# Optimization experiments

Hardware: AMD Instinct MI355X
Metric: run time of the kernel (lower is better)

## Reference

```python
import jax, jax.numpy as jnp
import numpy as np

B, L, D, I = 4, 4096, 2048, 5632


def setup_inputs() -> dict:
    key = jax.random.key(0)
    ks = jax.random.split(key, 8)
    s = 0.02  # weight init scale
    return {
        "hidden_states": jax.random.normal(ks[0], (B, L, D), dtype=jnp.float32),
        "gen_token_mask": jax.random.bernoulli(ks[1], 0.5, (B, L)),
        "und_gate": jax.random.normal(ks[2], (D, I), dtype=jnp.float32) * s,
        "und_up": jax.random.normal(ks[3], (D, I), dtype=jnp.float32) * s,
        "und_down": jax.random.normal(ks[4], (I, D), dtype=jnp.float32) * s,
        "gen_gate": jax.random.normal(ks[5], (D, I), dtype=jnp.float32) * s,
        "gen_up": jax.random.normal(ks[6], (D, I), dtype=jnp.float32) * s,
        "gen_down": jax.random.normal(ks[7], (I, D), dtype=jnp.float32) * s,
    }


def _swiglu_mlp(x, w_gate, w_up, w_down):
    # Qwen2MLP: down_proj(silu(gate_proj(x)) * up_proj(x)), no biases
    return jnp.einsum("bli,id->bld", jax.nn.silu(jnp.einsum("bld,di->bli", x, w_gate)) * jnp.einsum("bld,di->bli", x, w_up), w_down)


def reference(hidden_states, gen_token_mask, und_gate, und_up, und_down, gen_gate, gen_up, gen_down):
    # moe_forward: tokens with mask=True go to gen expert, others to und expert.
    # The torch code does gather->expert->scatter; the math is a per-token select
    # between the two experts' outputs, expressed here jit-compatibly as a where.
    und_out = _swiglu_mlp(hidden_states, und_gate, und_up, und_down)
    gen_out = _swiglu_mlp(hidden_states, gen_gate, gen_up, gen_down)
    return jnp.where(gen_token_mask[..., None], gen_out, und_out)
```

## Files before the change

### kernel.cpp

```cpp
#include <hip/hip_runtime.h>
#include <stdint.h>

#define D_DIM 2048
#define I_DIM 5632
#define NTOK  16384
#define MROWS 16512
#define MTILES 129
#define CH0   65
#define CH1   64
#define HROWS (CH0 * 128)

using f32x4  = __attribute__((ext_vector_type(4))) float;
using bf16x8 = __attribute__((ext_vector_type(8))) __bf16;
using u16x8  = __attribute__((ext_vector_type(8))) unsigned short;
using u16x4  = __attribute__((ext_vector_type(4))) unsigned short;
typedef unsigned short ushort;

__device__ __forceinline__ ushort f2bf(float f) {
  union { float f; unsigned int u; } v; v.f = f;
  unsigned int r = v.u + 0x7fffu + ((v.u >> 16) & 1u);
  return (ushort)(r >> 16);
}

__device__ __forceinline__ void glds16(const void* g, void* l) {
  __builtin_amdgcn_global_load_lds(
      (__attribute__((address_space(1))) void*)(g),
      (__attribute__((address_space(3))) void*)(l),
      16, 0, 0);
}

__global__ void count_kernel(const int* __restrict__ mask, int* __restrict__ cnt) {
  int i = blockIdx.x * 256 + threadIdx.x;
  if (i < NTOK && mask[i] == 0) atomicAdd(&cnt[0], 1);
}

__global__ void assign_kernel(const int* __restrict__ mask, int* __restrict__ cnt,
                              int* __restrict__ rowmap) {
  int i = blockIdx.x * 256 + threadIdx.x;
  if (i >= NTOK) return;
  int n0  = cnt[0];
  int n0p = (n0 + 127) & ~127;
  int row;
  if (mask[i] == 0) row = atomicAdd(&cnt[1], 1);
  else              row = n0p + atomicAdd(&cnt[2], 1);
  rowmap[row] = i;
}

__global__ __launch_bounds__(256) void cast_x_kernel(const float* __restrict__ in,
                                                     ushort* __restrict__ out) {
  int i = blockIdx.x * 256 + threadIdx.x;
  f32x4 v = ((const f32x4*)in)[i];
  u16x4 o;
#pragma unroll
  for (int j = 0; j < 4; j++) o[j] = f2bf(v[j]);
  ((u16x4*)out)[i] = o;
}

__global__ __launch_bounds__(256) void transpose_cast_kernel(
    const float* __restrict__ in, ushort* __restrict__ out, int R, int C) {
  __shared__ ushort s[64][72];
  int tC = blockIdx.x, tR = blockIdx.y;
  int tid = threadIdx.x;
  int r0 = tid >> 4;
  int c4 = (tid & 15) * 4;
  const float* src = in + (size_t)(tR * 64 + r0) * C + tC * 64 + c4;
#pragma unroll
  for (int rr = 0; rr < 64; rr += 16) {
    f32x4 v = *(const f32x4*)(src + (size_t)rr * C);
#pragma unroll
    for (int j = 0; j < 4; j++) s[r0 + rr][c4 + j] = f2bf(v[j]);
  }
  __syncthreads();
  int r8 = tid >> 3;
  int c8 = (tid & 7) * 8;
#pragma unroll
  for (int rr = 0; rr < 64; rr += 32) {
    int orow = r8 + rr;
    u16x8 v;
#pragma unroll
    for (int j = 0; j < 8; j++) v[j] = s[c8 + j][orow];
    *(u16x8*)(out + (size_t)(tC * 64 + orow) * R + tR * 64 + c8) = v;
  }
}

__global__ __launch_bounds__(256, 2)
void gateup_kernel(const ushort* __restrict__ x, const int* __restrict__ rowmap,
                   const int* __restrict__ cnt, const ushort* __restrict__ wt,
                   ushort* __restrict__ h, int mbase) {
  __shared__ ushort sA[128 * 64];
  __shared__ ushort sG[128 * 64];
  __shared__ ushort sU[128 * 64];

  const int bn = blockIdx.x, bm = blockIdx.y;
  const int gtile = mbase + bm;
  const int tid = threadIdx.x;
  const int lane = tid & 63, wave = tid >> 6;
  const int wm = (wave & 1) * 64, wn = (wave >> 1) * 64;
  const int lrow = lane & 15, quad = lane >> 4;

  const int n0p = (cnt[0] + 127) & ~127;
  const int grp = (gtile * 128 >= n0p) ? 1 : 0;
  const size_t WSZ = (size_t)I_DIM * D_DIM;
  const ushort* Wg = wt + (size_t)(grp * 2) * WSZ;
  const ushort* Wu = Wg + WSZ;

  const ushort *aP[4], *gP[4], *uP[4];
#pragma unroll
  for (int is = 0; is < 4; is++) {
    int g = is * 256 + tid;
    int r = g >> 3, c = g & 7;
    int cs = c ^ (r & 7);
    int tok = rowmap[gtile * 128 + r];
    if (tok < 0) tok = 0;
    aP[is] = x  + (size_t)tok * D_DIM + cs * 8;
    gP[is] = Wg + (size_t)(bn * 128 + r) * D_DIM + cs * 8;
    uP[is] = Wu + (size_t)(bn * 128 + r) * D_DIM + cs * 8;
  }

  f32x4 accG[4][4], accU[4][4];
#pragma unroll
  for (int i = 0; i < 4; i++)
#pragma unroll
    for (int j = 0; j < 4; j++) {
      accG[i][j] = (f32x4){0.f, 0.f, 0.f, 0.f};
      accU[i][j] = (f32x4){0.f, 0.f, 0.f, 0.f};
    }

  for (int k0 = 0; k0 < D_DIM; k0 += 64) {
#pragma unroll
    for (int is = 0; is < 4; is++) {
      int wbase = (is * 256 + wave * 64) * 8;
      glds16(aP[is] + k0, &sA[wbase]);
      glds16(gP[is] + k0, &sG[wbase]);
      glds16(uP[is] + k0, &sU[wbase]);
    }
    __syncthreads();
#pragma unroll
    for (int kk = 0; kk < 2; kk++) {
      const int co = ((kk * 4 + quad) ^ (lane & 7)) * 8;
      bf16x8 af[4], gf[4], uf[4];
#pragma unroll
      for (int i = 0; i < 4; i++) af[i] = *(const bf16x8*)&sA[(wm + i * 16 + lrow) * 64 + co];
#pragma unroll
      for (int j = 0; j < 4; j++) gf[j] = *(const bf16x8*)&sG[(wn + j * 16 + lrow) * 64 + co];
#pragma unroll
      for (int j = 0; j < 4; j++) uf[j] = *(const bf16x8*)&sU[(wn + j * 16 + lrow) * 64 + co];
#pragma unroll
      for (int i = 0; i < 4; i++)
#pragma unroll
        for (int j = 0; j < 4; j++) {
          accG[i][j] = __builtin_amdgcn_mfma_f32_16x16x32_bf16(af[i], gf[j], accG[i][j], 0, 0, 0);
          accU[i][j] = __builtin_amdgcn_mfma_f32_16x16x32_bf16(af[i], uf[j], accU[i][j], 0, 0, 0);
        }
    }
    __syncthreads();
  }

#pragma unroll
  for (int i = 0; i < 4; i++) {
    int rbase = bm * 128 + wm + i * 16 + quad * 4;
#pragma unroll
    for (int j = 0; j < 4; j++) {
      int col = bn * 128 + wn + j * 16 + lrow;
#pragma unroll
      for (int r = 0; r < 4; r++) {
        float g = accG[i][j][r];
        float u = accU[i][j][r];
        float s = g / (1.f + __expf(-g));
        h[(size_t)(rbase + r) * I_DIM + col] = f2bf(s * u);
      }
    }
  }
}

__global__ __launch_bounds__(256, 2)
void down_kernel(const ushort* __restrict__ h, const int* __restrict__ rowmap,
                 const int* __restrict__ cnt, const ushort* __restrict__ wdt,
                 float* __restrict__ out, int mbase) {
  __shared__ ushort sA[128 * 64];
  __shared__ ushort sB[128 * 64];

  const int bn = blockIdx.x, bm = blockIdx.y;
  const int gtile = mbase + bm;
  const int tid = threadIdx.x;
  const int lane = tid & 63, wave = tid >> 6;
  const int wm = (wave & 1) * 64, wn = (wave >> 1) * 64;
  const int lrow = lane & 15, quad = lane >> 4;

  const int n0p = (cnt[0] + 127) & ~127;
  const int grp = (gtile * 128 >= n0p) ? 1 : 0;
  const ushort* W = wdt + (size_t)grp * ((size_t)D_DIM * I_DIM);

  const ushort *aP[4], *bP[4];
#pragma unroll
  for (int is = 0; is < 4; is++) {
    int g = is * 256 + tid;
    int r = g >> 3, c = g & 7;
    int cs = c ^ (r & 7);
    aP[is] = h + (size_t)(bm * 128 + r) * I_DIM + cs * 8;
    bP[is] = W + (size_t)(bn * 128 + r) * I_DIM + cs * 8;
  }

  f32x4 acc[4][4];
#pragma unroll
  for (int i = 0; i < 4; i++)
#pragma unroll
    for (int j = 0; j < 4; j++) acc[i][j] = (f32x4){0.f, 0.f, 0.f, 0.f};

  for (int k0 = 0; k0 < I_DIM; k0 += 64) {
#pragma unroll
    for (int is = 0; is < 4; is++) {
      int wbase = (is * 256 + wave * 64) * 8;
      glds16(aP[is] + k0, &sA[wbase]);
      glds16(bP[is] + k0, &sB[wbase]);
    }
    __syncthreads();
#pragma unroll
    for (int kk = 0; kk < 2; kk++) {
      const int co = ((kk * 4 + quad) ^ (lane & 7)) * 8;
      bf16x8 af[4], bf[4];
#pragma unroll
      for (int i = 0; i < 4; i++) af[i] = *(const bf16x8*)&sA[(wm + i * 16 + lrow) * 64 + co];
#pragma unroll
      for (int j = 0; j < 4; j++) bf[j] = *(const bf16x8*)&sB[(wn + j * 16 + lrow) * 64 + co];
#pragma unroll
      for (int i = 0; i < 4; i++)
#pragma unroll
        for (int j = 0; j < 4; j++)
          acc[i][j] = __builtin_amdgcn_mfma_f32_16x16x32_bf16(af[i], bf[j], acc[i][j], 0, 0, 0);
    }
    __syncthreads();
  }

#pragma unroll
  for (int i = 0; i < 4; i++) {
    int rbase = gtile * 128 + wm + i * 16 + quad * 4;
#pragma unroll
    for (int r = 0; r < 4; r++) {
      int tok = rowmap[rbase + r];
      if (tok < 0) continue;
#pragma unroll
      for (int j = 0; j < 4; j++) {
        int col = bn * 128 + wn + j * 16 + lrow;
        out[(size_t)tok * D_DIM + col] = acc[i][j][r];
      }
    }
  }
}

extern "C" void kernel_launch(void* const* d_in, const int* in_sizes, int n_in,
                              void* d_out, int out_size, void* d_ws, size_t ws_size,
                              hipStream_t stream) {
  const float* x   = (const float*)d_in[0];
  const int* mask  = (const int*)d_in[1];
  const float* ug  = (const float*)d_in[2];
  const float* uu  = (const float*)d_in[3];
  const float* ud  = (const float*)d_in[4];
  const float* gg  = (const float*)d_in[5];
  const float* gu  = (const float*)d_in[6];
  const float* gd  = (const float*)d_in[7];
  float* out = (float*)d_out;

  char* ws = (char*)d_ws;
  int* cnt    = (int*)ws;
  int* rowmap = (int*)(ws + 256);
  ushort* xb  = (ushort*)(ws + 256 + 66048);
  ushort* wt  = xb + (size_t)NTOK * D_DIM;
  const size_t WSZ = (size_t)I_DIM * D_DIM;
  ushort* hbuf = wt + 6 * WSZ;

  hipMemsetAsync(cnt, 0, 256, stream);
  hipMemsetAsync(rowmap, 0xFF, MROWS * sizeof(int), stream);
  count_kernel<<<64, 256, 0, stream>>>(mask, cnt);
  assign_kernel<<<64, 256, 0, stream>>>(mask, cnt, rowmap);

  cast_x_kernel<<<(NTOK * D_DIM / 4) / 256, 256, 0, stream>>>(x, xb);

  transpose_cast_kernel<<<dim3(88, 32), 256, 0, stream>>>(ug, wt + 0 * WSZ, 2048, 5632);
  transpose_cast_kernel<<<dim3(88, 32), 256, 0, stream>>>(uu, wt + 1 * WSZ, 2048, 5632);
  transpose_cast_kernel<<<dim3(88, 32), 256, 0, stream>>>(gg, wt + 2 * WSZ, 2048, 5632);
  transpose_cast_kernel<<<dim3(88, 32), 256, 0, stream>>>(gu, wt + 3 * WSZ, 2048, 5632);
  transpose_cast_kernel<<<dim3(32, 88), 256, 0, stream>>>(ud, wt + 4 * WSZ, 5632, 2048);
  transpose_cast_kernel<<<dim3(32, 88), 256, 0, stream>>>(gd, wt + 5 * WSZ, 5632, 2048);

  gateup_kernel<<<dim3(I_DIM / 128, CH0), 256, 0, stream>>>(xb, rowmap, cnt, wt, hbuf, 0);
  down_kernel<<<dim3(D_DIM / 128, CH0), 256, 0, stream>>>(hbuf, rowmap, cnt, wt + 4 * WSZ, out, 0);
  gateup_kernel<<<dim3(I_DIM / 128, CH1), 256, 0, stream>>>(xb, rowmap, cnt, wt, hbuf, CH0);
  down_kernel<<<dim3(D_DIM / 128, CH1), 256, 0, stream>>>(hbuf, rowmap, cnt, wt + 4 * WSZ, out, CH0);
}
```

Measured before the change: 1.711 ms.

## Use 256x256 8-wave GEMM tiles with double-buffered LDS pipeline and interleaved gate/up weights

Replaces the 128x128 4-wave gate/up and down GEMMs with 256x256 tiles on 512-thread blocks. The LDS is double-buffered and the global-to-LDS prefetch is split into quarters, with explicit waitcnt, barriers and setprio to overlap loads with MFMA. Gate and up weights are interleaved in 16-row groups at transpose time, so one B tile serves both projections. Expert groups are now padded to 256 rows and the work is split into three chunks instead of two. The larger tiles cut global traffic per FLOP and the loop overhead, at the cost of more padding rows, higher register and LDS pressure (128KB per block) and fewer blocks for a wave-quantized grid.

```diff
diff --git a/kernel.cpp b/kernel.cpp
--- a/kernel.cpp
+++ b/kernel.cpp
@@ -4,11 +4,10 @@
 #define D_DIM 2048
 #define I_DIM 5632
 #define NTOK  16384
-#define MROWS 16512
-#define MTILES 129
-#define CH0   65
-#define CH1   64
-#define HROWS (CH0 * 128)
+#define NTILE 65
+#define MROWS (NTILE * 256)
+#define CHT   22
+#define HROWS (CHT * 256)
 
 using f32x4  = __attribute__((ext_vector_type(4))) float;
 using bf16x8 = __attribute__((ext_vector_type(8))) __bf16;
@@ -39,7 +38,7 @@
   int i = blockIdx.x * 256 + threadIdx.x;
   if (i >= NTOK) return;
   int n0  = cnt[0];
-  int n0p = (n0 + 127) & ~127;
+  int n0p = (n0 + 255) & ~255;
   int row;
   if (mask[i] == 0) row = atomicAdd(&cnt[1], 1);
   else              row = n0p + atomicAdd(&cnt[2], 1);
@@ -57,7 +56,7 @@
 }
 
 __global__ __launch_bounds__(256) void transpose_cast_kernel(
-    const float* __restrict__ in, ushort* __restrict__ out, int R, int C) {
+    const float* __restrict__ in, ushort* __restrict__ out, int R, int C, int phase) {
   __shared__ ushort s[64][72];
   int tC = blockIdx.x, tR = blockIdx.y;
   int tid = threadIdx.x;
@@ -79,169 +78,264 @@
     u16x8 v;
 #pragma unroll
     for (int j = 0; j < 8; j++) v[j] = s[c8 + j][orow];
-    *(u16x8*)(out + (size_t)(tC * 64 + orow) * R + tR * 64 + c8) = v;
-  }
-}
-
-__global__ __launch_bounds__(256, 2)
-void gateup_kernel(const ushort* __restrict__ x, const int* __restrict__ rowmap,
-                   const int* __restrict__ cnt, const ushort* __restrict__ wt,
-                   ushort* __restrict__ h, int mbase) {
-  __shared__ ushort sA[128 * 64];
-  __shared__ ushort sG[128 * 64];
-  __shared__ ushort sU[128 * 64];
+    int grow = tC * 64 + orow;
+    int irow = (phase >= 0) ? (((grow >> 4) * 2 + phase) * 16 + (grow & 15)) : grow;
+    *(u16x8*)(out + (size_t)irow * R + tR * 64 + c8) = v;
+  }
+}
+
+
+__global__ __launch_bounds__(512, 2)
+void gateup8_kernel(const ushort* __restrict__ x, const int* __restrict__ rowmap,
+                    const int* __restrict__ cnt, const ushort* __restrict__ wt,
+                    ushort* __restrict__ h, int mbase) {
+  __shared__ ushort sA[2][256 * 64];
+  __shared__ ushort sB[2][256 * 64];
 
   const int bn = blockIdx.x, bm = blockIdx.y;
   const int gtile = mbase + bm;
-  const int tid = threadIdx.x;
+  const int tid  = threadIdx.x;
   const int lane = tid & 63, wave = tid >> 6;
-  const int wm = (wave & 1) * 64, wn = (wave >> 1) * 64;
+  const int wm = wave >> 2, wn = wave & 3;
   const int lrow = lane & 15, quad = lane >> 4;
 
-  const int n0p = (cnt[0] + 127) & ~127;
-  const int grp = (gtile * 128 >= n0p) ? 1 : 0;
-  const size_t WSZ = (size_t)I_DIM * D_DIM;
-  const ushort* Wg = wt + (size_t)(grp * 2) * WSZ;
-  const ushort* Wu = Wg + WSZ;
-
-  const ushort *aP[4], *gP[4], *uP[4];
-#pragma unroll
-  for (int is = 0; is < 4; is++) {
-    int g = is * 256 + tid;
-    int r = g >> 3, c = g & 7;
-    int cs = c ^ (r & 7);
-    int tok = rowmap[gtile * 128 + r];
-    if (tok < 0) tok = 0;
-    aP[is] = x  + (size_t)tok * D_DIM + cs * 8;
-    gP[is] = Wg + (size_t)(bn * 128 + r) * D_DIM + cs * 8;
-    uP[is] = Wu + (size_t)(bn * 128 + r) * D_DIM + cs * 8;
-  }
-
-  f32x4 accG[4][4], accU[4][4];
-#pragma unroll
-  for (int i = 0; i < 4; i++)
-#pragma unroll
-    for (int j = 0; j < 4; j++) {
-      accG[i][j] = (f32x4){0.f, 0.f, 0.f, 0.f};
-      accU[i][j] = (f32x4){0.f, 0.f, 0.f, 0.f};
-    }
-
-  for (int k0 = 0; k0 < D_DIM; k0 += 64) {
-#pragma unroll
-    for (int is = 0; is < 4; is++) {
-      int wbase = (is * 256 + wave * 64) * 8;
-      glds16(aP[is] + k0, &sA[wbase]);
-      glds16(gP[is] + k0, &sG[wbase]);
-      glds16(uP[is] + k0, &sU[wbase]);
-    }
-    __syncthreads();
-#pragma unroll
-    for (int kk = 0; kk < 2; kk++) {
-      const int co = ((kk * 4 + quad) ^ (lane & 7)) * 8;
-      bf16x8 af[4], gf[4], uf[4];
-#pragma unroll
-      for (int i = 0; i < 4; i++) af[i] = *(const bf16x8*)&sA[(wm + i * 16 + lrow) * 64 + co];
-#pragma unroll
-      for (int j = 0; j < 4; j++) gf[j] = *(const bf16x8*)&sG[(wn + j * 16 + lrow) * 64 + co];
-#pragma unroll
-      for (int j = 0; j < 4; j++) uf[j] = *(const bf16x8*)&sU[(wn + j * 16 + lrow) * 64 + co];
-#pragma unroll
-      for (int i = 0; i < 4; i++)
+  const int n0p = (cnt[0] + 255) & ~255;
+  const int grp = (gtile * 256 >= n0p) ? 1 : 0;
+  const ushort* W = wt + (size_t)grp * (2 * (size_t)I_DIM * D_DIM);
+
+  const ushort* aSrc[2][2];
+  const ushort* bSrc[2][2];
+  int ldsOff[2][2];
+#pragma unroll
+  for (int hh = 0; hh < 2; hh++)
+#pragma unroll
+    for (int j = 0; j < 2; j++) {
+      int g = j * 512 + tid;
+      int r = g >> 3, c = g & 7;
+      int cs = c ^ (r & 7);
+      int tok = rowmap[gtile * 256 + hh * 128 + r];
+      if (tok < 0) tok = 0;
+      aSrc[hh][j] = x + (size_t)tok * D_DIM + cs * 8;
+      bSrc[hh][j] = W + (size_t)(bn * 256 + hh * 128 + r) * D_DIM + cs * 8;
+      ldsOff[hh][j] = hh * 8192 + (j * 512 + wave * 64) * 8;
+    }
+
+  f32x4 acc[8][4];
+#pragma unroll
+  for (int i = 0; i < 8; i++)
+#pragma unroll
+    for (int j = 0; j < 4; j++) acc[i][j] = (f32x4){0.f, 0.f, 0.f, 0.f};
+
+  constexpr int NT = D_DIM / 64;
+
+#pragma unroll
+  for (int hh = 0; hh < 2; hh++)
+#pragma unroll
+    for (int j = 0; j < 2; j++) glds16(aSrc[hh][j], &sA[0][ldsOff[hh][j]]);
+#pragma unroll
+  for (int hh = 0; hh < 2; hh++)
+#pragma unroll
+    for (int j = 0; j < 2; j++) glds16(bSrc[hh][j], &sB[0][ldsOff[hh][j]]);
+#pragma unroll
+  for (int hh = 0; hh < 2; hh++)
+#pragma unroll
+    for (int j = 0; j < 2; j++) glds16(bSrc[hh][j] + 64, &sB[1][ldsOff[hh][j]]);
+  asm volatile("s_waitcnt vmcnt(4)" ::: "memory");
+  __builtin_amdgcn_s_barrier();
+
+  bf16x8 bfr[4][2];
+  for (int t = 0; t < NT; ++t) {
+    const int cur  = t & 1;
+    const int kA   = ((t + 1 < NT) ? (t + 1) : (NT - 1)) * 64;
+    const int kB   = ((t + 2 < NT) ? (t + 2) : (NT - 1)) * 64;
+    const int bufA = cur ^ 1;
+#pragma unroll
+    for (int q = 0; q < 4; ++q) {
+      bf16x8 af[2][2];
+#pragma unroll
+      for (int mi = 0; mi < 2; mi++)
+#pragma unroll
+        for (int kk = 0; kk < 2; kk++) {
+          int row = wm * 128 + (2 * q + mi) * 16 + lrow;
+          int co  = ((kk * 4 + quad) ^ (lrow & 7)) * 8;
+          af[mi][kk] = *(const bf16x8*)&sA[cur][row * 64 + co];
+        }
+      if (q == 0) {
+#pragma unroll
+        for (int j = 0; j < 4; j++)
+#pragma unroll
+          for (int kk = 0; kk < 2; kk++) {
+            int row = wn * 64 + j * 16 + lrow;
+            int co  = ((kk * 4 + quad) ^ (lrow & 7)) * 8;
+            bfr[j][kk] = *(const bf16x8*)&sB[cur][row * 64 + co];
+          }
+      }
+      if (q == 0)      { glds16(aSrc[0][0] + kA, &sA[bufA][ldsOff[0][0]]);
+                         glds16(aSrc[0][1] + kA, &sA[bufA][ldsOff[0][1]]); }
+      else if (q == 1) { glds16(aSrc[1][0] + kA, &sA[bufA][ldsOff[1][0]]);
+                         glds16(aSrc[1][1] + kA, &sA[bufA][ldsOff[1][1]]); }
+      else if (q == 2) { glds16(bSrc[0][0] + kB, &sB[cur][ldsOff[0][0]]);
+                         glds16(bSrc[0][1] + kB, &sB[cur][ldsOff[0][1]]); }
+      else             { glds16(bSrc[1][0] + kB, &sB[cur][ldsOff[1][0]]);
+                         glds16(bSrc[1][1] + kB, &sB[cur][ldsOff[1][1]]); }
+
+      __builtin_amdgcn_sched_barrier(0);
+      __builtin_amdgcn_s_barrier();
+      asm volatile("s_waitcnt lgkmcnt(0)" ::: "memory");
+      __builtin_amdgcn_sched_barrier(0);
+      __builtin_amdgcn_s_setprio(1);
+#pragma unroll
+      for (int mi = 0; mi < 2; mi++)
 #pragma unroll
         for (int j = 0; j < 4; j++) {
-          accG[i][j] = __builtin_amdgcn_mfma_f32_16x16x32_bf16(af[i], gf[j], accG[i][j], 0, 0, 0);
-          accU[i][j] = __builtin_amdgcn_mfma_f32_16x16x32_bf16(af[i], uf[j], accU[i][j], 0, 0, 0);
+          acc[2 * q + mi][j] = __builtin_amdgcn_mfma_f32_16x16x32_bf16(af[mi][0], bfr[j][0], acc[2 * q + mi][j], 0, 0, 0);
+          acc[2 * q + mi][j] = __builtin_amdgcn_mfma_f32_16x16x32_bf16(af[mi][1], bfr[j][1], acc[2 * q + mi][j], 0, 0, 0);
         }
-    }
-    __syncthreads();
-  }
-
-#pragma unroll
-  for (int i = 0; i < 4; i++) {
-    int rbase = bm * 128 + wm + i * 16 + quad * 4;
-#pragma unroll
-    for (int j = 0; j < 4; j++) {
-      int col = bn * 128 + wn + j * 16 + lrow;
+      __builtin_amdgcn_s_setprio(0);
+      __builtin_amdgcn_sched_barrier(0);
+      if (q == 3) asm volatile("s_waitcnt vmcnt(4)" ::: "memory");
+      __builtin_amdgcn_s_barrier();
+    }
+  }
+
+#pragma unroll
+  for (int i = 0; i < 8; i++) {
+    int rbase = bm * 256 + wm * 128 + i * 16 + quad * 4;
+#pragma unroll
+    for (int pr = 0; pr < 2; pr++) {
+      int icol = bn * 128 + wn * 32 + pr * 16 + lrow;
 #pragma unroll
       for (int r = 0; r < 4; r++) {
-        float g = accG[i][j][r];
-        float u = accU[i][j][r];
+        float g = acc[i][2 * pr][r];
+        float u = acc[i][2 * pr + 1][r];
         float s = g / (1.f + __expf(-g));
-        h[(size_t)(rbase + r) * I_DIM + col] = f2bf(s * u);
+        h[(size_t)(rbase + r) * I_DIM + icol] = f2bf(s * u);
       }
     }
   }
 }
 
-__global__ __launch_bounds__(256, 2)
-void down_kernel(const ushort* __restrict__ h, const int* __restrict__ rowmap,
-                 const int* __restrict__ cnt, const ushort* __restrict__ wdt,
-                 float* __restrict__ out, int mbase) {
-  __shared__ ushort sA[128 * 64];
-  __shared__ ushort sB[128 * 64];
+__global__ __launch_bounds__(512, 2)
+void down8_kernel(const ushort* __restrict__ h, const int* __restrict__ rowmap,
+                  const int* __restrict__ cnt, const ushort* __restrict__ wdt,
+                  float* __restrict__ out, int mbase) {
+  __shared__ ushort sA[2][256 * 64];
+  __shared__ ushort sB[2][256 * 64];
 
   const int bn = blockIdx.x, bm = blockIdx.y;
   const int gtile = mbase + bm;
-  const int tid = threadIdx.x;
+  const int tid  = threadIdx.x;
   const int lane = tid & 63, wave = tid >> 6;
-  const int wm = (wave & 1) * 64, wn = (wave >> 1) * 64;
+  const int wm = wave >> 2, wn = wave & 3;
   const int lrow = lane & 15, quad = lane >> 4;
 
-  const int n0p = (cnt[0] + 127) & ~127;
-  const int grp = (gtile * 128 >= n0p) ? 1 : 0;
+  const int n0p = (cnt[0] + 255) & ~255;
+  const int grp = (gtile * 256 >= n0p) ? 1 : 0;
   const ushort* W = wdt + (size_t)grp * ((size_t)D_DIM * I_DIM);
 
-  const ushort *aP[4], *bP[4];
-#pragma unroll
-  for (int is = 0; is < 4; is++) {
-    int g = is * 256 + tid;
-    int r = g >> 3, c = g & 7;
-    int cs = c ^ (r & 7);
-    aP[is] = h + (size_t)(bm * 128 + r) * I_DIM + cs * 8;
-    bP[is] = W + (size_t)(bn * 128 + r) * I_DIM + cs * 8;
-  }
-
-  f32x4 acc[4][4];
-#pragma unroll
-  for (int i = 0; i < 4; i++)
+  const ushort* aSrc[2][2];
+  const ushort* bSrc[2][2];
+  int ldsOff[2][2];
+#pragma unroll
+  for (int hh = 0; hh < 2; hh++)
+#pragma unroll
+    for (int j = 0; j < 2; j++) {
+      int g = j * 512 + tid;
+      int r = g >> 3, c = g & 7;
+      int cs = c ^ (r & 7);
+      aSrc[hh][j] = h + (size_t)(bm * 256 + hh * 128 + r) * I_DIM + cs * 8;
+      bSrc[hh][j] = W + (size_t)(bn * 256 + hh * 128 + r) * I_DIM + cs * 8;
+      ldsOff[hh][j] = hh * 8192 + (j * 512 + wave * 64) * 8;
+    }
+
+  f32x4 acc[8][4];
+#pragma unroll
+  for (int i = 0; i < 8; i++)
 #pragma unroll
     for (int j = 0; j < 4; j++) acc[i][j] = (f32x4){0.f, 0.f, 0.f, 0.f};
 
-  for (int k0 = 0; k0 < I_DIM; k0 += 64) {
-#pragma unroll
-    for (int is = 0; is < 4; is++) {
-      int wbase = (is * 256 + wave * 64) * 8;
-      glds16(aP[is] + k0, &sA[wbase]);
-      glds16(bP[is] + k0, &sB[wbase]);
-    }
-    __syncthreads();
-#pragma unroll
-    for (int kk = 0; kk < 2; kk++) {
-      const int co = ((kk * 4 + quad) ^ (lane & 7)) * 8;
-      bf16x8 af[4], bf[4];
-#pragma unroll
-      for (int i = 0; i < 4; i++) af[i] = *(const bf16x8*)&sA[(wm + i * 16 + lrow) * 64 + co];
-#pragma unroll
-      for (int j = 0; j < 4; j++) bf[j] = *(const bf16x8*)&sB[(wn + j * 16 + lrow) * 64 + co];
-#pragma unroll
-      for (int i = 0; i < 4; i++)
+  constexpr int NT = I_DIM / 64;
+
+#pragma unroll
+  for (int hh = 0; hh < 2; hh++)
+#pragma unroll
+    for (int j = 0; j < 2; j++) glds16(aSrc[hh][j], &sA[0][ldsOff[hh][j]]);
+#pragma unroll
+  for (int hh = 0; hh < 2; hh++)
+#pragma unroll
+    for (int j = 0; j < 2; j++) glds16(bSrc[hh][j], &sB[0][ldsOff[hh][j]]);
+#pragma unroll
+  for (int hh = 0; hh < 2; hh++)
+#pragma unroll
+    for (int j = 0; j < 2; j++) glds16(bSrc[hh][j] + 64, &sB[1][ldsOff[hh][j]]);
+  asm volatile("s_waitcnt vmcnt(4)" ::: "memory");
+  __builtin_amdgcn_s_barrier();
+
+  bf16x8 bfr[4][2];
+  for (int t = 0; t < NT; ++t) {
+    const int cur  = t & 1;
+    const int kA   = ((t + 1 < NT) ? (t + 1) : (NT - 1)) * 64;
+    const int kB   = ((t + 2 < NT) ? (t + 2) : (NT - 1)) * 64;
+    const int bufA = cur ^ 1;
+#pragma unroll
+    for (int q = 0; q < 4; ++q) {
+      bf16x8 af[2][2];
+#pragma unroll
+      for (int mi = 0; mi < 2; mi++)
+#pragma unroll
+        for (int kk = 0; kk < 2; kk++) {
+          int row = wm * 128 + (2 * q + mi) * 16 + lrow;
+          int co  = ((kk * 4 + quad) ^ (lrow & 7)) * 8;
+          af[mi][kk] = *(const bf16x8*)&sA[cur][row * 64 + co];
+        }
+      if (q == 0) {
 #pragma unroll
         for (int j = 0; j < 4; j++)
-          acc[i][j] = __builtin_amdgcn_mfma_f32_16x16x32_bf16(af[i], bf[j], acc[i][j], 0, 0, 0);
-    }
-    __syncthreads();
-  }
-
-#pragma unroll
-  for (int i = 0; i < 4; i++) {
-    int rbase = gtile * 128 + wm + i * 16 + quad * 4;
+#pragma unroll
+          for (int kk = 0; kk < 2; kk++) {
+            int row = wn * 64 + j * 16 + lrow;
+            int co  = ((kk * 4 + quad) ^ (lrow & 7)) * 8;
+            bfr[j][kk] = *(const bf16x8*)&sB[cur][row * 64 + co];
+          }
+      }
+      if (q == 0)      { glds16(aSrc[0][0] + kA, &sA[bufA][ldsOff[0][0]]);
+                         glds16(aSrc[0][1] + kA, &sA[bufA][ldsOff[0][1]]); }
+      else if (q == 1) { glds16(aSrc[1][0] + kA, &sA[bufA][ldsOff[1][0]]);
+                         glds16(aSrc[1][1] + kA, &sA[bufA][ldsOff[1][1]]); }
+      else if (q == 2) { glds16(bSrc[0][0] + kB, &sB[cur][ldsOff[0][0]]);
+                         glds16(bSrc[0][1] + kB, &sB[cur][ldsOff[0][1]]); }
+      else             { glds16(bSrc[1][0] + kB, &sB[cur][ldsOff[1][0]]);
+                         glds16(bSrc[1][1] + kB, &sB[cur][ldsOff[1][1]]); }
+
+      __builtin_amdgcn_sched_barrier(0);
+      __builtin_amdgcn_s_barrier();
+      asm volatile("s_waitcnt lgkmcnt(0)" ::: "memory");
+      __builtin_amdgcn_sched_barrier(0);
+      __builtin_amdgcn_s_setprio(1);
+#pragma unroll
+      for (int mi = 0; mi < 2; mi++)
+#pragma unroll
+        for (int j = 0; j < 4; j++) {
+          acc[2 * q + mi][j] = __builtin_amdgcn_mfma_f32_16x16x32_bf16(af[mi][0], bfr[j][0], acc[2 * q + mi][j], 0, 0, 0);
+          acc[2 * q + mi][j] = __builtin_amdgcn_mfma_f32_16x16x32_bf16(af[mi][1], bfr[j][1], acc[2 * q + mi][j], 0, 0, 0);
+        }
+      __builtin_amdgcn_s_setprio(0);
+      __builtin_amdgcn_sched_barrier(0);
+      if (q == 3) asm volatile("s_waitcnt vmcnt(4)" ::: "memory");
+      __builtin_amdgcn_s_barrier();
+    }
+  }
+
+#pragma unroll
+  for (int i = 0; i < 8; i++) {
+    int grow = gtile * 256 + wm * 128 + i * 16 + quad * 4;
 #pragma unroll
     for (int r = 0; r < 4; r++) {
-      int tok = rowmap[rbase + r];
+      int tok = rowmap[grow + r];
       if (tok < 0) continue;
 #pragma unroll
       for (int j = 0; j < 4; j++) {
-        int col = bn * 128 + wn + j * 16 + lrow;
+        int col = bn * 256 + wn * 64 + j * 16 + lrow;
         out[(size_t)tok * D_DIM + col] = acc[i][j][r];
       }
     }
@@ -264,9 +358,9 @@
   char* ws = (char*)d_ws;
   int* cnt    = (int*)ws;
   int* rowmap = (int*)(ws + 256);
-  ushort* xb  = (ushort*)(ws + 256 + 66048);
-  ushort* wt  = xb + (size_t)NTOK * D_DIM;
+  ushort* xb  = (ushort*)(ws + 256 + MROWS * sizeof(int));
   const size_t WSZ = (size_t)I_DIM * D_DIM;
+  ushort* wt   = xb + (size_t)NTOK * D_DIM;
   ushort* hbuf = wt + 6 * WSZ;
 
   hipMemsetAsync(cnt, 0, 256, stream);
@@ -276,15 +370,19 @@
 
   cast_x_kernel<<<(NTOK * D_DIM / 4) / 256, 256, 0, stream>>>(x, xb);
 
-  transpose_cast_kernel<<<dim3(88, 32), 256, 0, stream>>>(ug, wt + 0 * WSZ, 2048, 5632);
-  transpose_cast_kernel<<<dim3(88, 32), 256, 0, stream>>>(uu, wt + 1 * WSZ, 2048, 5632);
-  transpose_cast_kernel<<<dim3(88, 32), 256, 0, stream>>>(gg, wt + 2 * WSZ, 2048, 5632);
-  transpose_cast_kernel<<<dim3(88, 32), 256, 0, stream>>>(gu, wt + 3 * WSZ, 2048, 5632);
-  transpose_cast_kernel<<<dim3(32, 88), 256, 0, stream>>>(ud, wt + 4 * WSZ, 5632, 2048);
-  transpose_cast_kernel<<<dim3(32, 88), 256, 0, stream>>>(gd, wt + 5 * WSZ, 5632, 2048);
-
-  gateup_kernel<<<dim3(I_DIM / 128, CH0), 256, 0, stream>>>(xb, rowmap, cnt, wt, hbuf, 0);
-  down_kernel<<<dim3(D_DIM / 128, CH0), 256, 0, stream>>>(hbuf, rowmap, cnt, wt + 4 * WSZ, out, 0);
-  gateup_kernel<<<dim3(I_DIM / 128, CH1), 256, 0, stream>>>(xb, rowmap, cnt, wt, hbuf, CH0);
-  down_kernel<<<dim3(D_DIM / 128, CH1), 256, 0, stream>>>(hbuf, rowmap, cnt, wt + 4 * WSZ, out, CH0);
-}
+  transpose_cast_kernel<<<dim3(88, 32), 256, 0, stream>>>(ug, wt,           2048, 5632, 0);
+  transpose_cast_kernel<<<dim3(88, 32), 256, 0, stream>>>(uu, wt,           2048, 5632, 1);
+  transpose_cast_kernel<<<dim3(88, 32), 256, 0, stream>>>(gg, wt + 2 * WSZ, 2048, 5632, 0);
+  transpose_cast_kernel<<<dim3(88, 32), 256, 0, stream>>>(gu, wt + 2 * WSZ, 2048, 5632, 1);
+  transpose_cast_kernel<<<dim3(32, 88), 256, 0, stream>>>(ud, wt + 4 * WSZ, 5632, 2048, -1);
+  transpose_cast_kernel<<<dim3(32, 88), 256, 0, stream>>>(gd, wt + 5 * WSZ, 5632, 2048, -1);
+
+  const int bases[3] = {0, 22, 44};
+  const int sizes[3] = {22, 22, 21};
+  for (int c = 0; c < 3; c++) {
+    gateup8_kernel<<<dim3(I_DIM * 2 / 256, sizes[c]), 512, 0, stream>>>(
+        xb, rowmap, cnt, wt, hbuf, bases[c]);
+    down8_kernel<<<dim3(D_DIM / 256, sizes[c]), 512, 0, stream>>>(
+        hbuf, rowmap, cnt, wt + 4 * WSZ, out, bases[c]);
+  }
+}
```

Measured after the change: 2.113 ms. +23.5%, slower.
